# Performance work log

Measured on AMD Instinct MI355X. Metric: run time of the kernel, lower is better.

The kernel has to match this reference:

```python
import jax, jax.numpy as jnp
import numpy as np

BS, SEQ, DIM, L = 32, 256, 6, 400
NH, DM, DFF, DOUT = 2, 4, 16, 32
MAXA, ILEN = SEQ // 2 + 2, 20
THR, HW = 0.001, 2


def _layernorm(x, g, b):
    m = x.mean(-1, keepdims=True)
    v = ((x - m) ** 2).mean(-1, keepdims=True)
    return (x - m) * jax.lax.rsqrt(v + 1e-5) * g + b


def _get_max(t, ws):
    # non-overlapping window peak suppression: keep only per-window argmax value
    bs, Lt = t.shape
    nwin = Lt // ws
    w = t[:, :nwin * ws].reshape(bs, nwin, ws)
    oh = jax.nn.one_hot(jnp.argmax(w, axis=2), ws, dtype=t.dtype)
    return (w * oh).reshape(bs, nwin * ws)


def reference(x, imu_mask, imu_len, conv_w, conv_b, W_b1, b_b1, W_fc, b_fc,
              Wqkv, Wo, ln1_g, ln1_b, Wf1, bf1, Wf2, bf2, ln2_g, ln2_b,
              Wout, bout, Wd1, bd1, Wd2, bd2, Wa, ba):
    bs, seq, dim, l = x.shape
    N = bs * seq
    # --- CNN encoder: valid conv1d -> relu -> 2-bin mean pool -> (N,32,2) ---
    y = jax.lax.conv_general_dilated(x.reshape(N, dim, l), conv_w, (1,), 'VALID',
                                     dimension_numbers=('NCH', 'OIH', 'NCH'))
    y = jax.nn.relu(y + conv_b[None, :, None])  # (N,32,398)
    half = y.shape[-1] // 2
    pooled = jnp.stack([y[:, :, :half].mean(-1), y[:, :, half:2 * half].mean(-1)], -1)
    cnn_flat = pooled.reshape(N, -1)  # (N,64)
    bridge_out = jax.nn.sigmoid(cnn_flat @ W_b1 + b_b1)  # (N,4)
    # --- one-step forecasting loss -> data-dependent peaks ---
    forcast_in = bridge_out.reshape(bs, seq, DM)
    shft = jnp.pad(forcast_in, ((0, 0), (1, 0), (0, 0)))[:, :-1]
    fmask = jnp.ones_like(forcast_in).at[:, 0, :].set(0.0)
    fmask = (fmask * imu_mask[:, :, 0, 0][:, :, None]).reshape(N, DM)
    forcast = shft.reshape(N, DM) @ W_fc + b_fc
    floss = jnp.mean(jnp.square(forcast * fmask - forcast_in.reshape(N, DM) * fmask), axis=1)
    floss = floss.reshape(bs, seq)
    lmask = jnp.ones_like(floss).at[:, :2].set(0.0).at[:, -2:].set(0.0)
    floss = floss * ((floss > THR) * lmask)
    sel = _get_max(floss, 2 * HW)            # (bs,seq)
    sel2 = _get_max(sel[:, HW:], 2 * HW)     # (bs,seq-4)
    sel2 = jnp.pad(sel2, ((0, 0), (HW, 0)))
    if sel.shape[1] > sel2.shape[1]:
        sel2 = jnp.pad(sel2, ((0, 0), (0, HW)))
    seg_points = sel2 > 0
    last = jnp.clip(jnp.round(imu_len.astype(jnp.float32) / seq).astype(jnp.int32), 2, seq)
    # --- merge unit-length segments (vectorized equivalent of the while-loop) ---
    pos = jnp.arange(seq)
    point = seg_points & (pos[None] < last[:, None])
    bnd_next = jnp.pad(point, ((0, 0), (0, 1)))[:, 1:] | (pos[None] + 1 == last[:, None])
    kept = point & ~bnd_next                 # a boundary survives iff next segment len > 1
    seg_id = jnp.cumsum(kept, axis=1)
    valid_t = pos[None] < last[:, None]
    same = (seg_id[:, :, None] == seg_id[:, None, :]) & valid_t[:, :, None] & valid_t[:, None, :]
    attn_mask = jnp.where(same | jnp.eye(seq, dtype=bool)[None], 0.0, -jnp.inf)[:, None]
    # --- 1-layer post-norm transformer with block-diagonal mask ---
    hb = bridge_out.reshape(seq, bs, DM).transpose(1, 0, 2)  # faithful reshape order
    qkv = jnp.einsum('bsd,cde->cbse', hb, Wqkv)
    hd = DM // NH
    q, k, v = [t.reshape(bs, seq, NH, hd) for t in qkv]
    scores = jnp.einsum('bqhd,bkhd->bhqk', q, k) / np.sqrt(hd) + attn_mask
    attn = jax.nn.softmax(scores, axis=-1)
    ao = jnp.einsum('bhqk,bkhd->bqhd', attn, v).reshape(bs, seq, DM) @ Wo
    h1 = _layernorm(hb + ao, ln1_g, ln1_b)
    ff = jax.nn.relu(h1 @ Wf1 + bf1) @ Wf2 + bf2
    h2 = _layernorm(h1 + ff, ln2_g, ln2_b)
    tr_out = h2 @ Wout + bout                # (bs,seq,32)
    # --- per-segment atom embeddings, padded to MAXA slots ---
    n_kept = kept.sum(1)
    kp = jnp.sort(jnp.where(kept, pos[None], seq), axis=1)[:, :MAXA]
    a_idx = jnp.arange(MAXA)
    ends = jnp.where(a_idx[None] < n_kept[:, None], kp, last[:, None])
    starts = jnp.concatenate([jnp.zeros((bs, 1), ends.dtype), ends[:, :-1]], axis=1)
    atom_valid = (a_idx[None] <= n_kept[:, None]).astype(x.dtype)
    emb = jnp.take_along_axis(tr_out, jnp.clip(ends - 1, 0, seq - 1)[:, :, None], axis=1)
    atom_gen = (emb.reshape(-1, DOUT) @ Wa + ba).reshape(bs, MAXA, dim, ILEN)
    atom_gen = atom_gen * atom_valid[:, :, None, None]
    # --- per-segment nearest resample to ILEN via one batched gather ---
    xf = x.transpose(0, 2, 1, 3).reshape(bs, dim, seq * l)
    in_len = (ends - starts) * l
    idx = starts[:, :, None] * l + (jnp.arange(ILEN)[None, None] * in_len[:, :, None]) // ILEN
    idx = jnp.clip(idx, 0, seq * l - 1)
    seg_interp = xf[jnp.arange(bs)[:, None, None], :, idx]  # (bs,MAXA,ILEN,dim)
    seg_interp = seg_interp.transpose(0, 1, 3, 2) * atom_valid[:, :, None, None]
    # --- imu decoder ---
    imu_gen = (jax.nn.relu(bridge_out @ Wd1 + bd1) @ Wd2 + bd2).reshape(bs, seq, dim, l)
    return jnp.concatenate([imu_gen.ravel(), atom_gen.ravel(), seg_interp.ravel(),
                            forcast.ravel(), floss.ravel()])


def setup_inputs() -> dict:
    key = jax.random.key(0)
    ks = jax.random.split(key, 20)
    f32 = jnp.float32
    nrm = lambda k, s, sc: jax.random.normal(k, s, f32) * sc
    inp = {
        'x': nrm(ks[0], (BS, SEQ, DIM, L), 1.0),
        'imu_mask': jnp.ones((BS, SEQ, 1, 1), f32),
        'imu_len': jax.random.randint(ks[1], (BS,), SEQ * SEQ // 2, SEQ * SEQ),
        'conv_w': nrm(ks[2], (32, DIM, 3), 0.24),
        'conv_b': jnp.zeros((32,), f32),
        'W_b1': nrm(ks[3], (64, DM), 0.125),
        'b_b1': jnp.zeros((DM,), f32),
        'W_fc': nrm(ks[4], (DM, DM), 0.5),
        'b_fc': jnp.zeros((DM,), f32),
        'Wqkv': nrm(ks[5], (3, DM, DM), 0.5),
        'Wo': nrm(ks[6], (DM, DM), 0.5),
        'ln1_g': jnp.ones((DM,), f32), 'ln1_b': jnp.zeros((DM,), f32),
        'Wf1': nrm(ks[7], (DM, DFF), 0.5), 'bf1': jnp.zeros((DFF,), f32),
        'Wf2': nrm(ks[8], (DFF, DM), 0.25), 'bf2': jnp.zeros((DM,), f32),
        'ln2_g': jnp.ones((DM,), f32), 'ln2_b': jnp.zeros((DM,), f32),
        'Wout': nrm(ks[9], (DM, DOUT), 0.5), 'bout': jnp.zeros((DOUT,), f32),
        'Wd1': nrm(ks[10], (DM, 64), 0.5), 'bd1': jnp.zeros((64,), f32),
        'Wd2': nrm(ks[11], (64, DIM * L), 0.125), 'bd2': jnp.zeros((DIM * L,), f32),
        'Wa': nrm(ks[12], (DOUT, DIM * ILEN), 0.18), 'ba': jnp.zeros((DIM * ILEN,), f32),
    }
    return inp
```

## Files before the change

kernel.cpp:

```cpp
#include <hip/hip_runtime.h>
#include <math.h>

#define OFF_IMU  0
#define OFF_ATOM 19660800
#define OFF_SEG  20160000
#define OFF_FC   20659200
#define OFF_FL   20691968

#define WS_BRIDGE 0
#define WS_TR     32768
#define WS_SEGID  294912
#define WS_ENDS   303104
#define WS_STARTS 307264
#define WS_NK     311424

static __device__ __forceinline__ int imin(int a, int b) { return a < b ? a : b; }
static __device__ __forceinline__ int imax(int a, int b) { return a > b ? a : b; }

#define PK_FMA_LO(S, W, X) \
    asm("v_pk_fma_f32 %0, %1, %2, %0 op_sel:[0,0,0] op_sel_hi:[1,0,1]" \
        : "+v"(S) : "v"(W), "v"(X))
#define PK_FMA_HI(S, W, X) \
    asm("v_pk_fma_f32 %0, %1, %2, %0 op_sel:[0,1,0] op_sel_hi:[1,1,1]" \
        : "+v"(S) : "v"(W), "v"(X))

union F4 { float4 q; float2 h[2]; };

__global__ __launch_bounds__(256) void k1_conv_bridge(
    const float* __restrict__ x, const float* __restrict__ conv_w,
    const float* __restrict__ conv_b, const float* __restrict__ W_b1,
    const float* __restrict__ b_b1, float* __restrict__ bridge)
{
    __shared__ __align__(16) float xs[4][2424];
    __shared__ float pooledL[4][64];
    const int tid = threadIdx.x;
    const int n0 = blockIdx.x * 4;

    const int wv = tid >> 6;
    const int l  = tid & 63;
    const int pr = l & 15;
    const int hg = (l >> 4) & 1;
    const int q  = l >> 5;

    float2 W2[18];
    {
        const float* wa = conv_w + (2 * pr) * 18;
        const float* wb = wa + 18;
#pragma unroll
        for (int j = 0; j < 18; ++j) W2[j] = make_float2(wa[j], wb[j]);
    }
    const float2 cb2 = make_float2(conv_b[2 * pr], conv_b[2 * pr + 1]);

    const float* xn = x + (size_t)n0 * 2400;
    for (int i = tid; i < 2400; i += 256) {
        const float4 v = ((const float4*)xn)[i];
        const int smp = i / 600;
        const int r = i - smp * 600;
        const int ic = r / 100, t4 = (r - ic * 100) * 4;
        *(float4*)&xs[smp][ic * 404 + t4] = v;
    }
    if (tid < 96) {
        const int smp = tid / 24, r = tid - smp * 24;
        xs[smp][(r >> 2) * 404 + 400 + (r & 3)] = 0.0f;
    }
    __syncthreads();

    const float* rb = &xs[wv][hg * 200 + q * 100];
    float2 accMain = make_float2(0.0f, 0.0f);
    float2 extra   = make_float2(0.0f, 0.0f);

    float2 c01[6], c23[6];
#pragma unroll
    for (int ic = 0; ic < 6; ++ic) {
        const F4 f = *(const F4*)(rb + ic * 404);
        c01[ic] = f.h[0]; c23[ic] = f.h[1];
    }

    for (int g = 0; g < 4; ++g) {
#pragma unroll
        for (int u = 0; u < 6; ++u) {
            float2 S0 = cb2, S1 = cb2, S2 = cb2, S3 = cb2;
#pragma unroll
            for (int ic = 0; ic < 6; ++ic) {
                const F4 nf = *(const F4*)(rb + ic * 404 + (u + 1) * 4);
                const float2 n01 = nf.h[0];
                const float2 w0 = W2[ic * 3 + 0], w1 = W2[ic * 3 + 1], w2 = W2[ic * 3 + 2];
                PK_FMA_LO(S0, w0, c01[ic]); PK_FMA_HI(S0, w1, c01[ic]); PK_FMA_LO(S0, w2, c23[ic]);
                PK_FMA_HI(S1, w0, c01[ic]); PK_FMA_LO(S1, w1, c23[ic]); PK_FMA_HI(S1, w2, c23[ic]);
                PK_FMA_LO(S2, w0, c23[ic]); PK_FMA_HI(S2, w1, c23[ic]); PK_FMA_LO(S2, w2, n01);
                PK_FMA_HI(S3, w0, c23[ic]); PK_FMA_LO(S3, w1, n01);     PK_FMA_HI(S3, w2, n01);
                c01[ic] = n01; c23[ic] = nf.h[1];
            }
            accMain.x += fmaxf(S0.x, 0.f) + fmaxf(S1.x, 0.f) + fmaxf(S2.x, 0.f) + fmaxf(S3.x, 0.f);
            accMain.y += fmaxf(S0.y, 0.f) + fmaxf(S1.y, 0.f) + fmaxf(S2.y, 0.f) + fmaxf(S3.y, 0.f);
        }
        rb += 24;
    }

    {
        float2 S0 = cb2, S1 = cb2, S2 = cb2, S3 = cb2;
#pragma unroll
        for (int ic = 0; ic < 6; ++ic) {
            const F4 nf = *(const F4*)(rb + ic * 404 + 4);
            const float2 n01 = nf.h[0];
            const float2 w0 = W2[ic * 3 + 0], w1 = W2[ic * 3 + 1], w2 = W2[ic * 3 + 2];
            PK_FMA_LO(S0, w0, c01[ic]); PK_FMA_HI(S0, w1, c01[ic]); PK_FMA_LO(S0, w2, c23[ic]);
            PK_FMA_HI(S1, w0, c01[ic]); PK_FMA_LO(S1, w1, c23[ic]); PK_FMA_HI(S1, w2, c23[ic]);
            PK_FMA_LO(S2, w0, c23[ic]); PK_FMA_HI(S2, w1, c23[ic]); PK_FMA_LO(S2, w2, n01);
            PK_FMA_HI(S3, w0, c23[ic]); PK_FMA_LO(S3, w1, n01);     PK_FMA_HI(S3, w2, n01);
        }
        const float r0x = fmaxf(S0.x, 0.f), r0y = fmaxf(S0.y, 0.f);
        const float r1x = fmaxf(S1.x, 0.f), r1y = fmaxf(S1.y, 0.f);
        const float r2x = fmaxf(S2.x, 0.f), r2y = fmaxf(S2.y, 0.f);
        const float r3x = fmaxf(S3.x, 0.f), r3y = fmaxf(S3.y, 0.f);
        if (q == 0) {
            accMain.x += r0x + r1x + r2x + r3x;
            accMain.y += r0y + r1y + r2y + r3y;
        } else if (hg == 0) {
            accMain.x += r0x + r1x + r2x;  extra.x = r3x;
            accMain.y += r0y + r1y + r2y;  extra.y = r3y;
        } else {
            accMain.x += r0x + r1x;
            accMain.y += r0y + r1y;
        }
    }

    float2 tot;
    tot.x = accMain.x + __shfl_xor(accMain.x, 32);
    tot.y = accMain.y + __shfl_xor(accMain.y, 32);
    const float exx = __shfl_xor(extra.x, 16);
    const float exy = __shfl_xor(extra.y, 16);
    if (hg) { tot.x += exx; tot.y += exy; }
    if (q) {
        pooledL[wv][(2 * pr + 0) * 2 + hg] = tot.x * (1.0f / 199.0f);
        pooledL[wv][(2 * pr + 1) * 2 + hg] = tot.y * (1.0f / 199.0f);
    }
    __syncthreads();

    {
        const int s2 = tid >> 6, f = tid & 63;
        const float v = pooledL[s2][f];
        const float4 wb = *(const float4*)(W_b1 + f * 4);
        float p0 = v * wb.x, p1 = v * wb.y, p2 = v * wb.z, p3 = v * wb.w;
#pragma unroll
        for (int off = 1; off < 64; off <<= 1) {
            p0 += __shfl_xor(p0, off, 64);
            p1 += __shfl_xor(p1, off, 64);
            p2 += __shfl_xor(p2, off, 64);
            p3 += __shfl_xor(p3, off, 64);
        }
        if (f == 0) {
            float* bp = bridge + (size_t)(n0 + s2) * 4;
            bp[0] = 1.0f / (1.0f + __expf(-(p0 + b_b1[0])));
            bp[1] = 1.0f / (1.0f + __expf(-(p1 + b_b1[1])));
            bp[2] = 1.0f / (1.0f + __expf(-(p2 + b_b1[2])));
            bp[3] = 1.0f / (1.0f + __expf(-(p3 + b_b1[3])));
        }
    }
}

__global__ __launch_bounds__(256) void k23_forcast_seg(
    const float* __restrict__ bridge, const float* __restrict__ imu_mask,
    const float* __restrict__ W_fc, const float* __restrict__ b_fc,
    const int* __restrict__ imu_len, float* __restrict__ out,
    int* __restrict__ segid_ws, int* __restrict__ ends_ws,
    int* __restrict__ starts_ws, int* __restrict__ nk_ws)
{
    const int b = blockIdx.x, tid = threadIdx.x;
    const int n = b * 256 + tid;
    __shared__ float fl[256];
    __shared__ float sel[256];
    __shared__ float sp[256];
    __shared__ int pk[256];
    __shared__ int sc[2][256];
    __shared__ int kpl[256];

    float sh[4], cur[4];
#pragma unroll
    for (int j = 0; j < 4; ++j) {
        sh[j] = (tid == 0) ? 0.0f : bridge[(n - 1) * 4 + j];
        cur[j] = bridge[n * 4 + j];
    }
    const float fm = ((tid == 0) ? 0.0f : 1.0f) * imu_mask[n];
    float flv = 0.0f;
#pragma unroll
    for (int j = 0; j < 4; ++j) {
        float f = b_fc[j];
#pragma unroll
        for (int i = 0; i < 4; ++i) f = fmaf(sh[i], W_fc[i * 4 + j], f);
        out[OFF_FC + n * 4 + j] = f;
        const float d = (f - cur[j]) * fm;
        flv = fmaf(d, d, flv);
    }
    flv *= 0.25f;
    const bool lm = (tid >= 2) && (tid < 254);
    flv = (flv > 0.001f && lm) ? flv : 0.0f;
    out[OFF_FL + n] = flv;

    fl[tid] = flv;
    sp[tid] = 0.0f;
    __syncthreads();
    if (tid < 64) {
        const int base = tid * 4;
        float m = fl[base]; int idx = 0;
#pragma unroll
        for (int i = 1; i < 4; ++i) { float v = fl[base + i]; if (v > m) { m = v; idx = i; } }
#pragma unroll
        for (int i = 0; i < 4; ++i) sel[base + i] = (i == idx) ? m : 0.0f;
    }
    __syncthreads();
    if (tid < 63) {
        const int base = 2 + tid * 4;
        float m = sel[base]; int idx = 0;
#pragma unroll
        for (int i = 1; i < 4; ++i) { float v = sel[base + i]; if (v > m) { m = v; idx = i; } }
        sp[base + idx] = (m > 0.0f) ? 1.0f : 0.0f;
    }
    __syncthreads();
    int last = (int)rintf((float)imu_len[b] * (1.0f / 256.0f));
    last = imin(imax(last, 2), 256);
    const int point = ((sp[tid] > 0.0f) && (tid < last)) ? 1 : 0;
    pk[tid] = point;
    __syncthreads();
    const int pnext = (tid < 255) ? pk[tid + 1] : 0;
    const int bnd = pnext | ((tid + 1 == last) ? 1 : 0);
    const int kept = (point && !bnd) ? 1 : 0;
    __syncthreads();
    sc[0][tid] = kept;
    __syncthreads();
    int src = 0;
    for (int off = 1; off < 256; off <<= 1) {
        const int v = sc[src][tid] + ((tid >= off) ? sc[src][tid - off] : 0);
        sc[src ^ 1][tid] = v;
        __syncthreads();
        src ^= 1;
    }
    const int myid = sc[src][tid];
    segid_ws[b * 256 + tid] = myid;
    const int nk = sc[src][255];
    if (kept) kpl[myid - 1] = tid;
    __syncthreads();
    if (tid < 130) {
        ends_ws[b * 130 + tid] = (tid < nk) ? kpl[tid] : last;
        starts_ws[b * 130 + tid] = (tid == 0) ? 0 : ((tid - 1 < nk) ? kpl[tid - 1] : last);
    }
    if (tid == 0) nk_ws[b] = nk;
}

__global__ __launch_bounds__(256) void k4_attn(
    const float* __restrict__ bridge, const int* __restrict__ segid_ws,
    const int* __restrict__ imu_len,
    const float* __restrict__ Wqkv, const float* __restrict__ Wo,
    const float* __restrict__ ln1_g, const float* __restrict__ ln1_b,
    const float* __restrict__ Wf1, const float* __restrict__ bf1,
    const float* __restrict__ Wf2, const float* __restrict__ bf2,
    const float* __restrict__ ln2_g, const float* __restrict__ ln2_b,
    const float* __restrict__ Wout, const float* __restrict__ bout,
    float* __restrict__ tr_ws)
{
    const int b = blockIdx.x >> 3;
    const int chunk = blockIdx.x & 7;
    const int tid = threadIdx.x;
    __shared__ float kv[256][8];
    __shared__ int sid[256];
    __shared__ float part[32][8][8];
    {
        const int s2 = tid;
        const float4 h = *(const float4*)(bridge + (size_t)(s2 * 32 + b) * 4);
#pragma unroll
        for (int e = 0; e < 4; ++e) {
            kv[s2][e]     = h.x * Wqkv[16 + e] + h.y * Wqkv[20 + e] + h.z * Wqkv[24 + e] + h.w * Wqkv[28 + e];
            kv[s2][4 + e] = h.x * Wqkv[32 + e] + h.y * Wqkv[36 + e] + h.z * Wqkv[40 + e] + h.w * Wqkv[44 + e];
        }
        sid[s2] = segid_ws[b * 256 + s2];
    }
    __syncthreads();
    int last = (int)rintf((float)imu_len[b] * (1.0f / 256.0f));
    last = imin(imax(last, 2), 256);
    const int lq = tid & 31;
    const int jg = tid >> 5;
    const int sq = chunk * 32 + lq;
    {
        const float4 h = *(const float4*)(bridge + (size_t)(sq * 32 + b) * 4);
        float q[4];
#pragma unroll
        for (int e = 0; e < 4; ++e)
            q[e] = h.x * Wqkv[e] + h.y * Wqkv[4 + e] + h.z * Wqkv[8 + e] + h.w * Wqkv[12 + e];
        const bool vs = sq < last;
        const int ms = sid[sq];
        const float isq = 0.70710678118654752f;
        float m0 = -1e30f, l0 = 0.f, a00 = 0.f, a01 = 0.f;
        float m1 = -1e30f, l1 = 0.f, a10 = 0.f, a11 = 0.f;
#pragma unroll 4
        for (int jj = 0; jj < 32; ++jj) {
            const int j = jg * 32 + jj;
            const bool allowed = (j == sq) || (vs && (j < last) && (sid[j] == ms));
            const float sc0 = (q[0] * kv[j][0] + q[1] * kv[j][1]) * isq;
            const float sc1 = (q[2] * kv[j][2] + q[3] * kv[j][3]) * isq;
            {
                const float mn = allowed ? fmaxf(m0, sc0) : m0;
                const float c = __expf(m0 - mn);
                const float e = allowed ? __expf(sc0 - mn) : 0.0f;
                l0 = l0 * c + e; a00 = a00 * c + e * kv[j][4]; a01 = a01 * c + e * kv[j][5]; m0 = mn;
            }
            {
                const float mn = allowed ? fmaxf(m1, sc1) : m1;
                const float c = __expf(m1 - mn);
                const float e = allowed ? __expf(sc1 - mn) : 0.0f;
                l1 = l1 * c + e; a10 = a10 * c + e * kv[j][6]; a11 = a11 * c + e * kv[j][7]; m1 = mn;
            }
        }
        float* pp = part[lq][jg];
        pp[0] = m0; pp[1] = l0; pp[2] = a00; pp[3] = a01;
        pp[4] = m1; pp[5] = l1; pp[6] = a10; pp[7] = a11;
    }
    __syncthreads();
    if (tid < 32) {
        const int s = chunk * 32 + tid;
        float M0 = -1e30f, L0 = 0.f, A00 = 0.f, A01 = 0.f;
        float M1 = -1e30f, L1 = 0.f, A10 = 0.f, A11 = 0.f;
#pragma unroll
        for (int p = 0; p < 8; ++p) {
            const float* pp = part[tid][p];
            {
                const float mn = fmaxf(M0, pp[0]);
                const float c0 = __expf(M0 - mn), c1 = __expf(pp[0] - mn);
                L0 = L0 * c0 + pp[1] * c1; A00 = A00 * c0 + pp[2] * c1; A01 = A01 * c0 + pp[3] * c1; M0 = mn;
            }
            {
                const float mn = fmaxf(M1, pp[4]);
                const float c0 = __expf(M1 - mn), c1 = __expf(pp[4] - mn);
                L1 = L1 * c0 + pp[5] * c1; A10 = A10 * c0 + pp[6] * c1; A11 = A11 * c0 + pp[7] * c1; M1 = mn;
            }
        }
        const float4 h = *(const float4*)(bridge + (size_t)(s * 32 + b) * 4);
        const float hb0 = h.x, hb1 = h.y, hb2 = h.z, hb3 = h.w;
        float ao[4] = {A00 / L0, A01 / L0, A10 / L1, A11 / L1};
        float x1[4];
#pragma unroll
        for (int jj = 0; jj < 4; ++jj)
            x1[jj] = ao[0] * Wo[jj] + ao[1] * Wo[4 + jj] + ao[2] * Wo[8 + jj] + ao[3] * Wo[12 + jj];
        x1[0] += hb0; x1[1] += hb1; x1[2] += hb2; x1[3] += hb3;
        float mean = 0.25f * (x1[0] + x1[1] + x1[2] + x1[3]);
        float var = 0.f;
#pragma unroll
        for (int i = 0; i < 4; ++i) { float d = x1[i] - mean; var += d * d; }
        var *= 0.25f;
        const float rs1 = rsqrtf(var + 1e-5f);
        float h1v[4];
#pragma unroll
        for (int i = 0; i < 4; ++i) h1v[i] = (x1[i] - mean) * rs1 * ln1_g[i] + ln1_b[i];
        float o2[4] = {bf2[0], bf2[1], bf2[2], bf2[3]};
#pragma unroll
        for (int kk = 0; kk < 16; ++kk) {
            float t = bf1[kk];
#pragma unroll
            for (int i = 0; i < 4; ++i) t = fmaf(h1v[i], Wf1[i * 16 + kk], t);
            t = fmaxf(t, 0.0f);
#pragma unroll
            for (int jj = 0; jj < 4; ++jj) o2[jj] = fmaf(t, Wf2[kk * 4 + jj], o2[jj]);
        }
        float x2[4];
#pragma unroll
        for (int i = 0; i < 4; ++i) x2[i] = h1v[i] + o2[i];
        float mean2 = 0.25f * (x2[0] + x2[1] + x2[2] + x2[3]);
        float var2 = 0.f;
#pragma unroll
        for (int i = 0; i < 4; ++i) { float d = x2[i] - mean2; var2 += d * d; }
        var2 *= 0.25f;
        const float rs2 = rsqrtf(var2 + 1e-5f);
        float h2v[4];
#pragma unroll
        for (int i = 0; i < 4; ++i) h2v[i] = (x2[i] - mean2) * rs2 * ln2_g[i] + ln2_b[i];
        float* tp = tr_ws + ((size_t)(b * 256 + s)) * 32;
#pragma unroll
        for (int mm = 0; mm < 32; ++mm)
            tp[mm] = bout[mm] + h2v[0] * Wout[mm] + h2v[1] * Wout[32 + mm]
                   + h2v[2] * Wout[64 + mm] + h2v[3] * Wout[96 + mm];
    }
}

__global__ __launch_bounds__(128) void k5_atoms(
    const float* __restrict__ x, const float* __restrict__ tr_ws,
    const int* __restrict__ ends_ws, const int* __restrict__ starts_ws,
    const int* __restrict__ nk_ws,
    const float* __restrict__ Wa, const float* __restrict__ ba,
    float* __restrict__ out)
{
    const int a = blockIdx.x;
    const int b = blockIdx.y;
    const int tid = threadIdx.x;
    __shared__ float emb[32];
    const int e = ends_ws[b * 130 + a];
    const int st = starts_ws[b * 130 + a];
    const int nk = nk_ws[b];
    const float valid = (a <= nk) ? 1.0f : 0.0f;
    const int ec = imin(imax(e - 1, 0), 255);
    if (tid < 32) emb[tid] = tr_ws[((size_t)(b * 256 + ec)) * 32 + tid];
    __syncthreads();
    if (tid < 120) {
        float v = ba[tid];
#pragma unroll
        for (int f = 0; f < 32; ++f) v = fmaf(emb[f], Wa[f * 120 + tid], v);
        out[OFF_ATOM + ((size_t)(b * 130 + a)) * 120 + tid] = v * valid;
        const int d = tid / 20, i = tid % 20;
        const int ilen = (e - st) * 400;
        int idx = st * 400 + (i * ilen) / 20;
        idx = imin(imax(idx, 0), 102399);
        const int si = idx / 400, ti = idx % 400;
        const float px = x[(((size_t)b * 256 + si) * 6 + d) * 400 + ti];
        out[OFF_SEG + ((size_t)(b * 130 + a)) * 120 + tid] = px * valid;
    }
}

__global__ __launch_bounds__(256) void k6_imu(
    const float* __restrict__ bridge, const float* __restrict__ Wd1,
    const float* __restrict__ bd1, const float* __restrict__ Wd2,
    const float* __restrict__ bd2, float* __restrict__ out)
{
    __shared__ float hl[64 * 32];
    const int n0 = blockIdx.x * 32;
    const int mb = blockIdx.y;
    const int tid = threadIdx.x;
    for (int e = tid; e < 2048; e += 256) {
        const int f = e >> 5, i = e & 31;
        const float4 br = *(const float4*)(bridge + (size_t)(n0 + i) * 4);
        const float v = bd1[f] + br.x * Wd1[f] + br.y * Wd1[64 + f]
                      + br.z * Wd1[128 + f] + br.w * Wd1[192 + f];
        hl[f * 32 + i] = fmaxf(v, 0.0f);
    }
    __syncthreads();
    const int gm = tid & 63, gn = tid >> 6;
    const int m0 = mb * 256 + gm * 4;
    if (m0 >= 2400) return;
    float acc[8][4];
#pragma unroll
    for (int r = 0; r < 8; ++r)
#pragma unroll
        for (int c = 0; c < 4; ++c) acc[r][c] = 0.f;
#pragma unroll 4
    for (int f = 0; f < 64; ++f) {
        const float4 w4 = *(const float4*)&Wd2[(size_t)f * 2400 + m0];
        const float4 h0 = *(const float4*)&hl[f * 32 + gn * 8];
        const float4 h1 = *(const float4*)&hl[f * 32 + gn * 8 + 4];
        const float hv[8] = {h0.x, h0.y, h0.z, h0.w, h1.x, h1.y, h1.z, h1.w};
        const float wv[4] = {w4.x, w4.y, w4.z, w4.w};
#pragma unroll
        for (int r = 0; r < 8; ++r)
#pragma unroll
            for (int c = 0; c < 4; ++c) acc[r][c] = fmaf(hv[r], wv[c], acc[r][c]);
    }
    const float4 bb = *(const float4*)&bd2[m0];
#pragma unroll
    for (int r = 0; r < 8; ++r) {
        float4 o;
        o.x = acc[r][0] + bb.x; o.y = acc[r][1] + bb.y;
        o.z = acc[r][2] + bb.z; o.w = acc[r][3] + bb.w;
        *(float4*)&out[OFF_IMU + (size_t)(n0 + gn * 8 + r) * 2400 + m0] = o;
    }
}

extern "C" void kernel_launch(void* const* d_in, const int* in_sizes, int n_in,
                              void* d_out, int out_size, void* d_ws, size_t ws_size,
                              hipStream_t stream)
{
    const float* x        = (const float*)d_in[0];
    const float* imu_mask = (const float*)d_in[1];
    const int*   imu_len  = (const int*)  d_in[2];
    const float* conv_w   = (const float*)d_in[3];
    const float* conv_b   = (const float*)d_in[4];
    const float* W_b1     = (const float*)d_in[5];
    const float* b_b1     = (const float*)d_in[6];
    const float* W_fc     = (const float*)d_in[7];
    const float* b_fc     = (const float*)d_in[8];
    const float* Wqkv     = (const float*)d_in[9];
    const float* Wo       = (const float*)d_in[10];
    const float* ln1_g    = (const float*)d_in[11];
    const float* ln1_b    = (const float*)d_in[12];
    const float* Wf1      = (const float*)d_in[13];
    const float* bf1      = (const float*)d_in[14];
    const float* Wf2      = (const float*)d_in[15];
    const float* bf2      = (const float*)d_in[16];
    const float* ln2_g    = (const float*)d_in[17];
    const float* ln2_b    = (const float*)d_in[18];
    const float* Wout     = (const float*)d_in[19];
    const float* bout     = (const float*)d_in[20];
    const float* Wd1      = (const float*)d_in[21];
    const float* bd1      = (const float*)d_in[22];
    const float* Wd2      = (const float*)d_in[23];
    const float* bd2      = (const float*)d_in[24];
    const float* Wa       = (const float*)d_in[25];
    const float* ba       = (const float*)d_in[26];

    float* out = (float*)d_out;
    float* wsf = (float*)d_ws;
    int*   wsi = (int*)d_ws;

    float* bridge = wsf + WS_BRIDGE;
    float* tr_ws  = wsf + WS_TR;
    int* segid  = wsi + WS_SEGID;
    int* ends   = wsi + WS_ENDS;
    int* starts = wsi + WS_STARTS;
    int* nk     = wsi + WS_NK;

    k1_conv_bridge<<<2048, 256, 0, stream>>>(x, conv_w, conv_b, W_b1, b_b1, bridge);
    k23_forcast_seg<<<32, 256, 0, stream>>>(bridge, imu_mask, W_fc, b_fc, imu_len,
                                            out, segid, ends, starts, nk);
    k4_attn<<<256, 256, 0, stream>>>(bridge, segid, imu_len, Wqkv, Wo, ln1_g, ln1_b,
                                     Wf1, bf1, Wf2, bf2, ln2_g, ln2_b, Wout, bout, tr_ws);
    k5_atoms<<<dim3(130, 32), 128, 0, stream>>>(x, tr_ws, ends, starts, nk, Wa, ba, out);
    k6_imu<<<dim3(256, 10), 256, 0, stream>>>(bridge, Wd1, bd1, Wd2, bd2, out);
}
```

Baseline: 119.0 us.

## Fuse forecast/segmentation kernel into attention kernel with redundant per-block recompute

Merges the separate forecast-loss and segmentation kernel into the attention kernel. Each attention block now recomputes the peak selection and prefix-scan segment ids for its batch directly in shared memory, instead of reading them from a workspace buffer. This removes one kernel launch and the dependency gap between the two kernels, along with the segid global round trip. The cost is that the small segmentation work is repeated across the chunk blocks of each batch, and those blocks write identical values to the fc, floss, ends and starts outputs. Shared memory use per block also grows.

After: 115.8 us. 2.6% less time.

```diff
diff --git a/kernel.cpp b/kernel.cpp
--- a/kernel.cpp
+++ b/kernel.cpp
@@ -9,7 +9,6 @@
 
 #define WS_BRIDGE 0
 #define WS_TR     32768
-#define WS_SEGID  294912
 #define WS_ENDS   303104
 #define WS_STARTS 307264
 #define WS_NK     311424
@@ -84,15 +83,15 @@
             for (int ic = 0; ic < 6; ++ic) {
                 const F4 nf = *(const F4*)(rb + ic * 404 + (u + 1) * 4);
                 const float2 n01 = nf.h[0];
-                const float2 w0 = W2[ic * 3 + 0], w1 = W2[ic * 3 + 1], w2 = W2[ic * 3 + 2];
+                const float2 w0 = W2[ic*3+0], w1 = W2[ic*3+1], w2 = W2[ic*3+2];
                 PK_FMA_LO(S0, w0, c01[ic]); PK_FMA_HI(S0, w1, c01[ic]); PK_FMA_LO(S0, w2, c23[ic]);
                 PK_FMA_HI(S1, w0, c01[ic]); PK_FMA_LO(S1, w1, c23[ic]); PK_FMA_HI(S1, w2, c23[ic]);
                 PK_FMA_LO(S2, w0, c23[ic]); PK_FMA_HI(S2, w1, c23[ic]); PK_FMA_LO(S2, w2, n01);
                 PK_FMA_HI(S3, w0, c23[ic]); PK_FMA_LO(S3, w1, n01);     PK_FMA_HI(S3, w2, n01);
                 c01[ic] = n01; c23[ic] = nf.h[1];
             }
-            accMain.x += fmaxf(S0.x, 0.f) + fmaxf(S1.x, 0.f) + fmaxf(S2.x, 0.f) + fmaxf(S3.x, 0.f);
-            accMain.y += fmaxf(S0.y, 0.f) + fmaxf(S1.y, 0.f) + fmaxf(S2.y, 0.f) + fmaxf(S3.y, 0.f);
+            accMain.x += fmaxf(S0.x,0.f)+fmaxf(S1.x,0.f)+fmaxf(S2.x,0.f)+fmaxf(S3.x,0.f);
+            accMain.y += fmaxf(S0.y,0.f)+fmaxf(S1.y,0.f)+fmaxf(S2.y,0.f)+fmaxf(S3.y,0.f);
         }
         rb += 24;
     }
@@ -103,16 +102,16 @@
         for (int ic = 0; ic < 6; ++ic) {
             const F4 nf = *(const F4*)(rb + ic * 404 + 4);
             const float2 n01 = nf.h[0];
-            const float2 w0 = W2[ic * 3 + 0], w1 = W2[ic * 3 + 1], w2 = W2[ic * 3 + 2];
+            const float2 w0 = W2[ic*3+0], w1 = W2[ic*3+1], w2 = W2[ic*3+2];
             PK_FMA_LO(S0, w0, c01[ic]); PK_FMA_HI(S0, w1, c01[ic]); PK_FMA_LO(S0, w2, c23[ic]);
             PK_FMA_HI(S1, w0, c01[ic]); PK_FMA_LO(S1, w1, c23[ic]); PK_FMA_HI(S1, w2, c23[ic]);
             PK_FMA_LO(S2, w0, c23[ic]); PK_FMA_HI(S2, w1, c23[ic]); PK_FMA_LO(S2, w2, n01);
             PK_FMA_HI(S3, w0, c23[ic]); PK_FMA_LO(S3, w1, n01);     PK_FMA_HI(S3, w2, n01);
         }
-        const float r0x = fmaxf(S0.x, 0.f), r0y = fmaxf(S0.y, 0.f);
-        const float r1x = fmaxf(S1.x, 0.f), r1y = fmaxf(S1.y, 0.f);
-        const float r2x = fmaxf(S2.x, 0.f), r2y = fmaxf(S2.y, 0.f);
-        const float r3x = fmaxf(S3.x, 0.f), r3y = fmaxf(S3.y, 0.f);
+        const float r0x = fmaxf(S0.x,0.f), r0y = fmaxf(S0.y,0.f);
+        const float r1x = fmaxf(S1.x,0.f), r1y = fmaxf(S1.y,0.f);
+        const float r2x = fmaxf(S2.x,0.f), r2y = fmaxf(S2.y,0.f);
+        const float r3x = fmaxf(S3.x,0.f), r3y = fmaxf(S3.y,0.f);
         if (q == 0) {
             accMain.x += r0x + r1x + r2x + r3x;
             accMain.y += r0y + r1y + r2y + r3y;
@@ -159,97 +158,11 @@
     }
 }
 
-__global__ __launch_bounds__(256) void k23_forcast_seg(
+__global__ __launch_bounds__(256) void k234_seg_attn(
     const float* __restrict__ bridge, const float* __restrict__ imu_mask,
     const float* __restrict__ W_fc, const float* __restrict__ b_fc,
     const int* __restrict__ imu_len, float* __restrict__ out,
-    int* __restrict__ segid_ws, int* __restrict__ ends_ws,
-    int* __restrict__ starts_ws, int* __restrict__ nk_ws)
-{
-    const int b = blockIdx.x, tid = threadIdx.x;
-    const int n = b * 256 + tid;
-    __shared__ float fl[256];
-    __shared__ float sel[256];
-    __shared__ float sp[256];
-    __shared__ int pk[256];
-    __shared__ int sc[2][256];
-    __shared__ int kpl[256];
-
-    float sh[4], cur[4];
-#pragma unroll
-    for (int j = 0; j < 4; ++j) {
-        sh[j] = (tid == 0) ? 0.0f : bridge[(n - 1) * 4 + j];
-        cur[j] = bridge[n * 4 + j];
-    }
-    const float fm = ((tid == 0) ? 0.0f : 1.0f) * imu_mask[n];
-    float flv = 0.0f;
-#pragma unroll
-    for (int j = 0; j < 4; ++j) {
-        float f = b_fc[j];
-#pragma unroll
-        for (int i = 0; i < 4; ++i) f = fmaf(sh[i], W_fc[i * 4 + j], f);
-        out[OFF_FC + n * 4 + j] = f;
-        const float d = (f - cur[j]) * fm;
-        flv = fmaf(d, d, flv);
-    }
-    flv *= 0.25f;
-    const bool lm = (tid >= 2) && (tid < 254);
-    flv = (flv > 0.001f && lm) ? flv : 0.0f;
-    out[OFF_FL + n] = flv;
-
-    fl[tid] = flv;
-    sp[tid] = 0.0f;
-    __syncthreads();
-    if (tid < 64) {
-        const int base = tid * 4;
-        float m = fl[base]; int idx = 0;
-#pragma unroll
-        for (int i = 1; i < 4; ++i) { float v = fl[base + i]; if (v > m) { m = v; idx = i; } }
-#pragma unroll
-        for (int i = 0; i < 4; ++i) sel[base + i] = (i == idx) ? m : 0.0f;
-    }
-    __syncthreads();
-    if (tid < 63) {
-        const int base = 2 + tid * 4;
-        float m = sel[base]; int idx = 0;
-#pragma unroll
-        for (int i = 1; i < 4; ++i) { float v = sel[base + i]; if (v > m) { m = v; idx = i; } }
-        sp[base + idx] = (m > 0.0f) ? 1.0f : 0.0f;
-    }
-    __syncthreads();
-    int last = (int)rintf((float)imu_len[b] * (1.0f / 256.0f));
-    last = imin(imax(last, 2), 256);
-    const int point = ((sp[tid] > 0.0f) && (tid < last)) ? 1 : 0;
-    pk[tid] = point;
-    __syncthreads();
-    const int pnext = (tid < 255) ? pk[tid + 1] : 0;
-    const int bnd = pnext | ((tid + 1 == last) ? 1 : 0);
-    const int kept = (point && !bnd) ? 1 : 0;
-    __syncthreads();
-    sc[0][tid] = kept;
-    __syncthreads();
-    int src = 0;
-    for (int off = 1; off < 256; off <<= 1) {
-        const int v = sc[src][tid] + ((tid >= off) ? sc[src][tid - off] : 0);
-        sc[src ^ 1][tid] = v;
-        __syncthreads();
-        src ^= 1;
-    }
-    const int myid = sc[src][tid];
-    segid_ws[b * 256 + tid] = myid;
-    const int nk = sc[src][255];
-    if (kept) kpl[myid - 1] = tid;
-    __syncthreads();
-    if (tid < 130) {
-        ends_ws[b * 130 + tid] = (tid < nk) ? kpl[tid] : last;
-        starts_ws[b * 130 + tid] = (tid == 0) ? 0 : ((tid - 1 < nk) ? kpl[tid - 1] : last);
-    }
-    if (tid == 0) nk_ws[b] = nk;
-}
-
-__global__ __launch_bounds__(256) void k4_attn(
-    const float* __restrict__ bridge, const int* __restrict__ segid_ws,
-    const int* __restrict__ imu_len,
+    int* __restrict__ ends_ws, int* __restrict__ starts_ws, int* __restrict__ nk_ws,
     const float* __restrict__ Wqkv, const float* __restrict__ Wo,
     const float* __restrict__ ln1_g, const float* __restrict__ ln1_b,
     const float* __restrict__ Wf1, const float* __restrict__ bf1,
@@ -264,28 +177,105 @@
     __shared__ float kv[256][8];
     __shared__ int sid[256];
     __shared__ float part[32][8][8];
+    __shared__ float fl[256];
+    __shared__ float sel[256];
+    __shared__ float sp[256];
+    __shared__ int pk[256];
+    __shared__ int sc[2][256];
+    __shared__ int kpl[256];
+
     {
-        const int s2 = tid;
-        const float4 h = *(const float4*)(bridge + (size_t)(s2 * 32 + b) * 4);
+        const float4 h = *(const float4*)(bridge + (size_t)(tid * 32 + b) * 4);
 #pragma unroll
         for (int e = 0; e < 4; ++e) {
-            kv[s2][e]     = h.x * Wqkv[16 + e] + h.y * Wqkv[20 + e] + h.z * Wqkv[24 + e] + h.w * Wqkv[28 + e];
-            kv[s2][4 + e] = h.x * Wqkv[32 + e] + h.y * Wqkv[36 + e] + h.z * Wqkv[40 + e] + h.w * Wqkv[44 + e];
-        }
-        sid[s2] = segid_ws[b * 256 + s2];
+            kv[tid][e]     = h.x * Wqkv[16 + e] + h.y * Wqkv[20 + e] + h.z * Wqkv[24 + e] + h.w * Wqkv[28 + e];
+            kv[tid][4 + e] = h.x * Wqkv[32 + e] + h.y * Wqkv[36 + e] + h.z * Wqkv[40 + e] + h.w * Wqkv[44 + e];
+        }
+    }
+
+    {
+        const int n = b * 256 + tid;
+        float sh[4], cur[4];
+#pragma unroll
+        for (int j = 0; j < 4; ++j) {
+            sh[j] = (tid == 0) ? 0.0f : bridge[(n - 1) * 4 + j];
+            cur[j] = bridge[n * 4 + j];
+        }
+        const float fm = ((tid == 0) ? 0.0f : 1.0f) * imu_mask[n];
+        float flv = 0.0f;
+#pragma unroll
+        for (int j = 0; j < 4; ++j) {
+            float f = b_fc[j];
+#pragma unroll
+            for (int i = 0; i < 4; ++i) f = fmaf(sh[i], W_fc[i * 4 + j], f);
+            out[OFF_FC + n * 4 + j] = f;
+            const float d = (f - cur[j]) * fm;
+            flv = fmaf(d, d, flv);
+        }
+        flv *= 0.25f;
+        const bool lm = (tid >= 2) && (tid < 254);
+        flv = (flv > 0.001f && lm) ? flv : 0.0f;
+        out[OFF_FL + n] = flv;
+        fl[tid] = flv;
+        sp[tid] = 0.0f;
+    }
+    __syncthreads();
+
+    if (tid < 64) {
+        const int base = tid * 4;
+        float m = fl[base]; int idx = 0;
+#pragma unroll
+        for (int i = 1; i < 4; ++i) { float v = fl[base + i]; if (v > m) { m = v; idx = i; } }
+#pragma unroll
+        for (int i = 0; i < 4; ++i) sel[base + i] = (i == idx) ? m : 0.0f;
+    }
+    __syncthreads();
+    if (tid < 63) {
+        const int base = 2 + tid * 4;
+        float m = sel[base]; int idx = 0;
+#pragma unroll
+        for (int i = 1; i < 4; ++i) { float v = sel[base + i]; if (v > m) { m = v; idx = i; } }
+        sp[base + idx] = (m > 0.0f) ? 1.0f : 0.0f;
     }
     __syncthreads();
     int last = (int)rintf((float)imu_len[b] * (1.0f / 256.0f));
     last = imin(imax(last, 2), 256);
+    const int point = ((sp[tid] > 0.0f) && (tid < last)) ? 1 : 0;
+    pk[tid] = point;
+    __syncthreads();
+    const int pnext = (tid < 255) ? pk[tid + 1] : 0;
+    const int bnd = pnext | ((tid + 1 == last) ? 1 : 0);
+    const int kept = (point && !bnd) ? 1 : 0;
+    __syncthreads();
+    sc[0][tid] = kept;
+    __syncthreads();
+    int src = 0;
+    for (int off = 1; off < 256; off <<= 1) {
+        const int v = sc[src][tid] + ((tid >= off) ? sc[src][tid - off] : 0);
+        sc[src ^ 1][tid] = v;
+        __syncthreads();
+        src ^= 1;
+    }
+    const int myid = sc[src][tid];
+    sid[tid] = myid;
+    const int nk = sc[src][255];
+    if (kept) kpl[myid - 1] = tid;
+    __syncthreads();
+    if (tid < 130) {
+        ends_ws[b * 130 + tid] = (tid < nk) ? kpl[tid] : last;
+        starts_ws[b * 130 + tid] = (tid == 0) ? 0 : ((tid - 1 < nk) ? kpl[tid - 1] : last);
+    }
+    if (tid == 0) nk_ws[b] = nk;
+
     const int lq = tid & 31;
     const int jg = tid >> 5;
     const int sq = chunk * 32 + lq;
     {
         const float4 h = *(const float4*)(bridge + (size_t)(sq * 32 + b) * 4);
-        float q[4];
+        float qv[4];
 #pragma unroll
         for (int e = 0; e < 4; ++e)
-            q[e] = h.x * Wqkv[e] + h.y * Wqkv[4 + e] + h.z * Wqkv[8 + e] + h.w * Wqkv[12 + e];
+            qv[e] = h.x * Wqkv[e] + h.y * Wqkv[4 + e] + h.z * Wqkv[8 + e] + h.w * Wqkv[12 + e];
         const bool vs = sq < last;
         const int ms = sid[sq];
         const float isq = 0.70710678118654752f;
@@ -295,8 +285,8 @@
         for (int jj = 0; jj < 32; ++jj) {
             const int j = jg * 32 + jj;
             const bool allowed = (j == sq) || (vs && (j < last) && (sid[j] == ms));
-            const float sc0 = (q[0] * kv[j][0] + q[1] * kv[j][1]) * isq;
-            const float sc1 = (q[2] * kv[j][2] + q[3] * kv[j][3]) * isq;
+            const float sc0 = (qv[0] * kv[j][0] + qv[1] * kv[j][1]) * isq;
+            const float sc1 = (qv[2] * kv[j][2] + qv[3] * kv[j][3]) * isq;
             {
                 const float mn = allowed ? fmaxf(m0, sc0) : m0;
                 const float c = __expf(m0 - mn);
@@ -498,16 +488,15 @@
 
     float* bridge = wsf + WS_BRIDGE;
     float* tr_ws  = wsf + WS_TR;
-    int* segid  = wsi + WS_SEGID;
     int* ends   = wsi + WS_ENDS;
     int* starts = wsi + WS_STARTS;
     int* nk     = wsi + WS_NK;
 
     k1_conv_bridge<<<2048, 256, 0, stream>>>(x, conv_w, conv_b, W_b1, b_b1, bridge);
-    k23_forcast_seg<<<32, 256, 0, stream>>>(bridge, imu_mask, W_fc, b_fc, imu_len,
-                                            out, segid, ends, starts, nk);
-    k4_attn<<<256, 256, 0, stream>>>(bridge, segid, imu_len, Wqkv, Wo, ln1_g, ln1_b,
-                                     Wf1, bf1, Wf2, bf2, ln2_g, ln2_b, Wout, bout, tr_ws);
+    k234_seg_attn<<<256, 256, 0, stream>>>(bridge, imu_mask, W_fc, b_fc, imu_len,
+                                           out, ends, starts, nk,
+                                           Wqkv, Wo, ln1_g, ln1_b, Wf1, bf1,
+                                           Wf2, bf2, ln2_g, ln2_b, Wout, bout, tr_ws);
     k5_atoms<<<dim3(130, 32), 128, 0, stream>>>(x, tr_ws, ends, starts, nk, Wa, ba, out);
     k6_imu<<<dim3(256, 10), 256, 0, stream>>>(bridge, Wd1, bd1, Wd2, bd2, out);
 }
```
